# Performance work log

Measured on AMD Instinct MI355X. Metric: run time of the kernel, lower is better.

## Reference

```python
import jax, jax.numpy as jnp
import numpy as np

N = 50000      # num_nodes
E = 800000     # edges (before self loops)
IN = 64        # in_dim
H = 128        # hidden_node_dim
DH = 256       # decoder_and_message_hidden_dim
L = 3          # propagation_steps


def _lin(key, fan_in, fan_out):
    s = 1.0 / np.sqrt(fan_in)
    return jax.random.uniform(key, (fan_in, fan_out), jnp.float32, -s, s)


def setup_inputs() -> dict:
    key = jax.random.key(0)
    ks = iter(jax.random.split(key, 40))
    x = jax.random.normal(next(ks), (N, IN), jnp.float32)
    edge_index = jax.random.randint(next(ks), (2, E), 0, N, jnp.int64)
    enc_W = _lin(next(ks), IN, H); enc_b = jnp.zeros((H,), jnp.float32)
    # message MLP: Linear(2H->DH) tanh, Linear(DH->DH) tanh, Linear(DH->H)
    msg_W0 = jnp.stack([_lin(next(ks), 2 * H, DH) for _ in range(L)])
    msg_b0 = jnp.zeros((L, DH), jnp.float32)
    msg_W1 = jnp.stack([_lin(next(ks), DH, DH) for _ in range(L)])
    msg_b1 = jnp.zeros((L, DH), jnp.float32)
    msg_W2 = jnp.stack([_lin(next(ks), DH, H) for _ in range(L)])
    msg_b2 = jnp.zeros((L, H), jnp.float32)
    # GRUCell params, torch layout [3H, H] chunks (r, z, n)
    gru_Wih = jnp.stack([_lin(next(ks), H, 3 * H).T for _ in range(L)])
    gru_Whh = jnp.stack([_lin(next(ks), H, 3 * H).T for _ in range(L)])
    gru_bih = jnp.zeros((L, 3 * H), jnp.float32)
    gru_bhh = jnp.zeros((L, 3 * H), jnp.float32)
    # decoder: Linear(H->DH) tanh, Linear(DH->DH) tanh, Linear(DH->1)
    dec_W0 = _lin(next(ks), H, DH); dec_b0 = jnp.zeros((DH,), jnp.float32)
    dec_W1 = _lin(next(ks), DH, DH); dec_b1 = jnp.zeros((DH,), jnp.float32)
    dec_W2 = _lin(next(ks), DH, 1); dec_b2 = jnp.zeros((1,), jnp.float32)
    return dict(x=x, edge_index=edge_index, enc_W=enc_W, enc_b=enc_b,
                msg_W0=msg_W0, msg_b0=msg_b0, msg_W1=msg_W1, msg_b1=msg_b1,
                msg_W2=msg_W2, msg_b2=msg_b2, gru_Wih=gru_Wih, gru_Whh=gru_Whh,
                gru_bih=gru_bih, gru_bhh=gru_bhh, dec_W0=dec_W0, dec_b0=dec_b0,
                dec_W1=dec_W1, dec_b1=dec_b1, dec_W2=dec_W2, dec_b2=dec_b2)


def reference(x, edge_index, enc_W, enc_b, msg_W0, msg_b0, msg_W1, msg_b1,
              msg_W2, msg_b2, gru_Wih, gru_Whh, gru_bih, gru_bhh,
              dec_W0, dec_b0, dec_W1, dec_b1, dec_W2, dec_b2):
    n = x.shape[0]
    # add self loops (PyG add_self_loops appends (v, v))
    loops = jnp.arange(n, dtype=edge_index.dtype)
    src = jnp.concatenate([edge_index[0], loops])  # j (source)
    dst = jnp.concatenate([edge_index[1], loops])  # i (target)
    counts = jax.ops.segment_sum(jnp.ones_like(dst, jnp.float32), dst, num_segments=n)
    h = jnp.tanh(x @ enc_W + enc_b)                # encoder [N, H]
    for l in range(L):
        # message: f([x_i || x_j]) per edge
        m = jnp.concatenate([h[dst], h[src]], axis=-1)            # [E+N, 2H]
        m = jnp.tanh(m @ msg_W0[l] + msg_b0[l])
        m = jnp.tanh(m @ msg_W1[l] + msg_b1[l])
        m = m @ msg_W2[l] + msg_b2[l]                              # [E+N, H]
        aggr = jax.ops.segment_sum(m, dst, num_segments=n) / counts[:, None]
        # GRUCell(input=aggr, hidden=h)
        gi = aggr @ gru_Wih[l].T + gru_bih[l]                      # [N, 3H]
        gh = h @ gru_Whh[l].T + gru_bhh[l]
        i_r, i_z, i_n = jnp.split(gi, 3, axis=-1)
        h_r, h_z, h_n = jnp.split(gh, 3, axis=-1)
        r = jax.nn.sigmoid(i_r + h_r)
        z = jax.nn.sigmoid(i_z + h_z)
        nn_ = jnp.tanh(i_n + r * h_n)
        h = (1.0 - z) * nn_ + z * h
    # decoder
    y = jnp.tanh(h @ dec_W0 + dec_b0)
    y = jnp.tanh(y @ dec_W1 + dec_b1)
    y = y @ dec_W2 + dec_b2                                        # [N, 1]
    return y.reshape(-1, n)[0]                                     # view(-1, N).squeeze(0)
```

## Files before the change

### kernel.cpp

```cpp
#include <hip/hip_runtime.h>

typedef __bf16 bf16x8 __attribute__((ext_vector_type(8)));
typedef float  f32x4  __attribute__((ext_vector_type(4)));

__device__ inline unsigned short f2bf(float f){
  __bf16 b = (__bf16)f;
  return __builtin_bit_cast(unsigned short, b);
}
__device__ inline unsigned int pack2bf(float lo, float hi){
  return (unsigned)f2bf(lo) | ((unsigned)f2bf(hi) << 16);
}
__device__ inline float tanh_fast(float x){
  float e = __builtin_amdgcn_exp2f(x * 2.8853900817779268f);
  return 1.0f - 2.0f * __builtin_amdgcn_rcpf(e + 1.0f);
}
__device__ inline float sigmoid_fast(float x){
  float e = __builtin_amdgcn_exp2f(x * -1.4426950408889634f);
  return __builtin_amdgcn_rcpf(1.0f + e);
}
__device__ inline float bflo(unsigned int u){ return __uint_as_float(u << 16); }
__device__ inline float bfhi(unsigned int u){ return __uint_as_float(u & 0xffff0000u); }

__device__ __forceinline__ void bar_nodrain(){
  asm volatile("s_waitcnt lgkmcnt(0)" ::: "memory");
  __builtin_amdgcn_s_barrier();
}

__device__ inline int nthbit(unsigned long long m, int n){
  for (int k = 0; k < n; k++) m &= m - 1;
  return m ? (int)__builtin_ctzll(m) : 0;
}

__global__ void k_count(const int* __restrict__ ei, int* __restrict__ cnt, int E){
  int e = blockIdx.x * 256 + threadIdx.x;
  if (e < E) atomicAdd(&cnt[ei[E + e]], 1);
}

__global__ __launch_bounds__(1024) void k_scan(const int* __restrict__ cnt, int* __restrict__ cursor, int N){
  __shared__ int partial[1024];
  int t = threadIdx.x;
  int chunk = (N + 1023) / 1024;
  int lo = t * chunk, hi = min(lo + chunk, N);
  int s = 0;
  for (int v = lo; v < hi; v++) s += cnt[v] + 1;
  partial[t] = s;
  __syncthreads();
  for (int off = 1; off < 1024; off <<= 1){
    int val = (t >= off) ? partial[t - off] : 0;
    __syncthreads();
    partial[t] += val;
    __syncthreads();
  }
  int base = (t == 0) ? 0 : partial[t - 1];
  for (int v = lo; v < hi; v++){ cursor[v] = base; base += cnt[v] + 1; }
}

__global__ void k_scatter(const int* __restrict__ ei, int* __restrict__ cursor,
                          int* __restrict__ srcS, int* __restrict__ dstS, int E, int N){
  int i = blockIdx.x * 256 + threadIdx.x;
  int Et = E + N;
  if (i >= Et) return;
  int s, d;
  if (i < E){ s = ei[i]; d = ei[E + i]; } else { s = d = i - E; }
  int pos = atomicAdd(&cursor[d], 1);
  srcS[pos] = s; dstS[pos] = d;
}

__global__ void k_wprep(const float* __restrict__ msgW1, const float* __restrict__ msgW2,
                        unsigned short* __restrict__ W1T, unsigned short* __restrict__ W2T){
  int idx = blockIdx.x * 256 + threadIdx.x;
  if (idx < 3 * 256 * 256){
    int l = idx >> 16, r = idx & 65535; int n = r >> 8, k = r & 255;
    W1T[idx] = f2bf(msgW1[(size_t)l * 65536 + k * 256 + n]);
  }
  int i2 = idx - 3 * 65536;
  if (i2 >= 0 && i2 < 3 * 128 * 256){
    int l = i2 >> 15, r = i2 & 32767; int hh = r >> 8, k = r & 255;
    W2T[i2] = f2bf(msgW2[(size_t)l * 32768 + k * 128 + hh]);
  }
}

__global__ void k_wprep2(const float* __restrict__ msgW0, unsigned short* __restrict__ W0T){
  int idx = blockIdx.x * 256 + threadIdx.x;
  if (idx >= 3 * 2 * 256 * 128) return;
  int l = idx / 65536, r = idx % 65536;
  int half = r >> 15, r2 = r & 32767, c = r2 >> 7, k = r2 & 127;
  W0T[idx] = f2bf(msgW0[(size_t)l * 65536 + (half * 128 + k) * 256 + c]);
}

__global__ void k_wprep3(const float* __restrict__ gWih, const float* __restrict__ gWhh,
                         unsigned short* __restrict__ Wcat){
  int idx = blockIdx.x * 256 + threadIdx.x;
  if (idx >= 3 * 384 * 256) return;
  int l = idx / 98304, r = idx % 98304, j = r >> 8, k = r & 255;
  float v = (k < 128) ? gWih[((size_t)l * 384 + j) * 128 + k]
                      : gWhh[((size_t)l * 384 + j) * 128 + (k - 128)];
  Wcat[idx] = f2bf(v);
}

__global__ void k_wprep4(const float* __restrict__ encW, const float* __restrict__ dW0,
                         const float* __restrict__ dW1,
                         const float* __restrict__ gbih, const float* __restrict__ gbhh,
                         unsigned short* __restrict__ encWT, unsigned short* __restrict__ dW0T,
                         unsigned short* __restrict__ dW1T,
                         float* __restrict__ brz, float* __restrict__ bin, float* __restrict__ bhn){
  int idx = blockIdx.x * 256 + threadIdx.x;
  if (idx < 8192){ int c = idx >> 6, k = idx & 63; encWT[idx] = f2bf(encW[k * 128 + c]); return; }
  idx -= 8192;
  if (idx < 32768){ int c = idx >> 7, k = idx & 127; dW0T[idx] = f2bf(dW0[k * 256 + c]); return; }
  idx -= 32768;
  if (idx < 65536){ int c = idx >> 8, k = idx & 255; dW1T[idx] = f2bf(dW1[k * 256 + c]); return; }
  idx -= 65536;
  if (idx < 768){ int l = idx >> 8, j = idx & 255; brz[idx] = gbih[l * 384 + j] + gbhh[l * 384 + j]; return; }
  idx -= 768;
  if (idx < 384){ int l = idx >> 7, j = idx & 127; bin[idx] = gbih[l * 384 + 256 + j]; return; }
  idx -= 384;
  if (idx < 384){ int l = idx >> 7, j = idx & 127; bhn[idx] = gbhh[l * 384 + 256 + j]; return; }
}

__global__ __launch_bounds__(256) void k_enc(const float* __restrict__ x,
        const unsigned short* __restrict__ encWT, const float* __restrict__ encb,
        float* __restrict__ h, unsigned short* __restrict__ hb, int N){
  __shared__ __align__(16) unsigned char xb[64 * 128];
  int n0 = blockIdx.x * 64, t = threadIdx.x;
  #pragma unroll
  for (int p = 0; p < 2; p++){
    int i = t + p * 256;
    int row = i >> 3, ch = i & 7;
    int node = n0 + row;
    unsigned int o[4] = {0,0,0,0};
    if (node < N){
      const float* s = x + (size_t)node * 64 + ch * 8;
      float4 a = *(const float4*)s, b = *(const float4*)(s + 4);
      o[0] = pack2bf(a.x, a.y);
      o[1] = pack2bf(a.z, a.w);
      o[2] = pack2bf(b.x, b.y);
      o[3] = pack2bf(b.z, b.w);
    }
    *(uint4*)(xb + row * 128 + ((ch * 16) ^ ((row & 7) << 4))) = make_uint4(o[0], o[1], o[2], o[3]);
  }
  __syncthreads();
  int wv = t >> 6, lane = t & 63, l15 = lane & 15, kg = lane >> 4;
  int c32 = wv * 32;
  f32x4 acc[2][4];
  #pragma unroll
  for (int ct = 0; ct < 2; ct++){
    int c = c32 + ct * 16 + kg * 4;
    float4 be = *(const float4*)(encb + c);
    f32x4 binit = {be.x, be.y, be.z, be.w};
    #pragma unroll
    for (int b_ = 0; b_ < 4; b_++) acc[ct][b_] = binit;
  }
  const unsigned char* wp = (const unsigned char*)encWT;
  #pragma unroll
  for (int ks = 0; ks < 2; ks++){
    int koff = ks * 64 + kg * 16;
    bf16x8 bfr[4], afr[2];
    #pragma unroll
    for (int nt = 0; nt < 4; nt++){
      int row = nt * 16 + l15;
      bfr[nt] = *(const bf16x8*)(xb + row * 128 + (koff ^ ((row & 7) << 4)));
    }
    #pragma unroll
    for (int ct = 0; ct < 2; ct++)
      afr[ct] = *(const bf16x8*)(wp + (size_t)(c32 + ct * 16 + l15) * 128 + koff);
    #pragma unroll
    for (int ct = 0; ct < 2; ct++)
      #pragma unroll
      for (int nt = 0; nt < 4; nt++)
        acc[ct][nt] = __builtin_amdgcn_mfma_f32_16x16x32_bf16(afr[ct], bfr[nt], acc[ct][nt], 0, 0, 0);
  }
  #pragma unroll
  for (int ct = 0; ct < 2; ct++){
    int c = c32 + ct * 16 + kg * 4;
    #pragma unroll
    for (int nt = 0; nt < 4; nt++){
      int node = n0 + nt * 16 + l15;
      if (node >= N) continue;
      f32x4 v = acc[ct][nt];
      float o0 = tanh_fast(v[0]), o1 = tanh_fast(v[1]);
      float o2 = tanh_fast(v[2]), o3 = tanh_fast(v[3]);
      float4 fo; fo.x = o0; fo.y = o1; fo.z = o2; fo.w = o3;
      *(float4*)(h + (size_t)node * 128 + c) = fo;
      uint2 bo; bo.x = pack2bf(o0, o1); bo.y = pack2bf(o2, o3);
      *(uint2*)(hb + (size_t)node * 128 + c) = bo;
    }
  }
}

__global__ __launch_bounds__(256) void k_ab(const unsigned short* __restrict__ hb,
        const unsigned short* __restrict__ W0T, const float* __restrict__ b0,
        unsigned short* __restrict__ A, unsigned short* __restrict__ B, int N){
  __shared__ __align__(16) unsigned char ub[64 * 256];
  int n0 = blockIdx.x * 64, t = threadIdx.x;
  #pragma unroll
  for (int p = 0; p < 4; p++){
    int i = t + p * 256;
    int row = i >> 4, ch = i & 15;
    int node = n0 + row;
    uint4 v = (node < N) ? *(const uint4*)(hb + (size_t)node * 128 + ch * 8) : make_uint4(0,0,0,0);
    *(uint4*)(ub + row * 256 + ((ch * 16) ^ ((row & 7) << 4))) = v;
  }
  __syncthreads();
  int wv = t >> 6, lane = t & 63, l15 = lane & 15, kg = lane >> 4;
  f32x4 zero = {0.f, 0.f, 0.f, 0.f};
  int c64 = wv * 64;
  f32x4 accA[4][4], accB[4][4];
  #pragma unroll
  for (int ct = 0; ct < 4; ct++){
    int c = c64 + ct * 16 + kg * 4;
    float4 b4 = *(const float4*)(b0 + c);
    f32x4 binit = {b4.x, b4.y, b4.z, b4.w};
    #pragma unroll
    for (int b_ = 0; b_ < 4; b_++){ accA[ct][b_] = binit; accB[ct][b_] = zero; }
  }
  const unsigned char* wa = (const unsigned char*)W0T;
  const unsigned char* wb = wa + 65536;
  #pragma unroll
  for (int ks = 0; ks < 4; ks++){
    int koff = ks * 64 + kg * 16;
    bf16x8 bfr[4];
    #pragma unroll
    for (int nt = 0; nt < 4; nt++){
      int row = nt * 16 + l15;
      bfr[nt] = *(const bf16x8*)(ub + row * 256 + (koff ^ ((row & 7) << 4)));
    }
    bf16x8 afA[4], afB[4];
    #pragma unroll
    for (int ct = 0; ct < 4; ct++){
      int r = c64 + ct * 16 + l15;
      afA[ct] = *(const bf16x8*)(wa + (size_t)r * 256 + koff);
      afB[ct] = *(const bf16x8*)(wb + (size_t)r * 256 + koff);
    }
    #pragma unroll
    for (int ct = 0; ct < 4; ct++)
      #pragma unroll
      for (int nt = 0; nt < 4; nt++){
        accA[ct][nt] = __builtin_amdgcn_mfma_f32_16x16x32_bf16(afA[ct], bfr[nt], accA[ct][nt], 0, 0, 0);
        accB[ct][nt] = __builtin_amdgcn_mfma_f32_16x16x32_bf16(afB[ct], bfr[nt], accB[ct][nt], 0, 0, 0);
      }
  }
  #pragma unroll
  for (int ct = 0; ct < 4; ct++){
    int c = c64 + ct * 16 + kg * 4;
    #pragma unroll
    for (int nt = 0; nt < 4; nt++){
      int node = n0 + nt * 16 + l15;
      if (node >= N) continue;
      f32x4 va = accA[ct][nt], vb = accB[ct][nt];
      uint2 oa, ob;
      oa.x = pack2bf(va[0], va[1]); oa.y = pack2bf(va[2], va[3]);
      ob.x = pack2bf(vb[0], vb[1]); ob.y = pack2bf(vb[2], vb[3]);
      *(uint2*)(A + (size_t)node * 256 + c) = oa;
      *(uint2*)(B + (size_t)node * 256 + c) = ob;
    }
  }
}

__global__ __launch_bounds__(256, 4) void k_edge(
        const int* __restrict__ srcS, const int* __restrict__ dstS,
        const unsigned short* __restrict__ Abuf, const unsigned short* __restrict__ Bbuf,
        const unsigned short* __restrict__ W1T, const unsigned short* __restrict__ W2T,
        const float* __restrict__ b1, const float* __restrict__ b2,
        float* __restrict__ aggr){
  __shared__ __align__(16) unsigned char lds[40960];
  unsigned char* t0  = lds;
  unsigned char* t1q = lds + 32768;
  int t = threadIdx.x;
  int wv = t >> 6, lane = t & 63, l15 = lane & 15, kg = lane >> 4;
  int e0 = blockIdx.x * 64;

  int sv = srcS[e0 + lane];
  int dv = dstS[e0 + lane];

  int chunk = lane & 31;
  int rbase = wv * 2 + (lane >> 5);
  uint4 av[8], bv[8];
  #pragma unroll
  for (int p = 0; p < 8; p++){
    int row = p * 8 + rbase;
    int d = __shfl(dv, row), s = __shfl(sv, row);
    if (d >= 0){
      av[p] = *(const uint4*)(Abuf + (size_t)d * 256 + chunk * 8);
      bv[p] = *(const uint4*)(Bbuf + (size_t)s * 256 + chunk * 8);
    } else { av[p] = make_uint4(0,0,0,0); bv[p] = make_uint4(0,0,0,0); }
  }

  int prevd = __shfl(dv, (lane == 0) ? 0 : (lane - 1));
  bool valid = (dv >= 0);
  bool flag  = valid && (lane == 0 || prevd != dv);
  unsigned long long sm  = __ballot(flag);
  unsigned long long ivm = __ballot(!valid);
  int nseg   = (int)__popcll(sm);
  int endAll = 64 - (int)__popcll(ivm);

  int segSt, segEn, segD;
  {
    int st_ = nthbit(sm, lane);
    int en_ = (lane + 1 < nseg) ? nthbit(sm, lane + 1) : endAll;
    segSt = st_; segEn = en_;
    segD  = __shfl(dv, st_);
  }

  #pragma unroll
  for (int p = 0; p < 8; p++){
    int r = p * 8 + rbase;
    unsigned int o[4]; unsigned int ua, ub;
    ua = av[p].x; ub = bv[p].x;
    o[0] = pack2bf(tanh_fast(bflo(ua)+bflo(ub)), tanh_fast(bfhi(ua)+bfhi(ub)));
    ua = av[p].y; ub = bv[p].y;
    o[1] = pack2bf(tanh_fast(bflo(ua)+bflo(ub)), tanh_fast(bfhi(ua)+bfhi(ub)));
    ua = av[p].z; ub = bv[p].z;
    o[2] = pack2bf(tanh_fast(bflo(ua)+bflo(ub)), tanh_fast(bfhi(ua)+bfhi(ub)));
    ua = av[p].w; ub = bv[p].w;
    o[3] = pack2bf(tanh_fast(bflo(ua)+bflo(ub)), tanh_fast(bfhi(ua)+bfhi(ub)));
    *(uint4*)(t0 + r * 512 + ((chunk * 16) ^ ((r & 7) << 4))) = make_uint4(o[0],o[1],o[2],o[3]);
  }
  bar_nodrain();

  const unsigned char* w1b = (const unsigned char*)W1T;
  const unsigned char* w2b = (const unsigned char*)W2T;
  int hbase = wv * 32;

  f32x4 acc2[2][4];
  #pragma unroll
  for (int ht = 0; ht < 2; ht++){
    int hb_ = hbase + ht * 16 + kg * 4;
    float4 c4 = *(const float4*)(b2 + hb_);
    f32x4 binit = {c4.x, c4.y, c4.z, c4.w};
    #pragma unroll
    for (int b_ = 0; b_ < 4; b_++) acc2[ht][b_] = binit;
  }

  #pragma unroll
  for (int pass = 0; pass < 4; pass++){
    {
      int nbase = pass * 64 + wv * 16;
      f32x4 acc[4];
      {
        int ng = nbase + kg * 4;
        float4 c4 = *(const float4*)(b1 + ng);
        f32x4 binit = {c4.x, c4.y, c4.z, c4.w};
        #pragma unroll
        for (int b_ = 0; b_ < 4; b_++) acc[b_] = binit;
      }
      #pragma unroll
      for (int ks = 0; ks < 8; ks++){
        int koff = ks * 64 + kg * 16;
        bf16x8 afr = *(const bf16x8*)(w1b + (size_t)(nbase + l15) * 512 + koff);
        bf16x8 bfr[4];
        #pragma unroll
        for (int et = 0; et < 4; et++){
          int row = et * 16 + l15;
          bfr[et] = *(const bf16x8*)(t0 + row * 512 + (koff ^ ((row & 7) << 4)));
        }
        #pragma unroll
        for (int et = 0; et < 4; et++)
          acc[et] = __builtin_amdgcn_mfma_f32_16x16x32_bf16(afr, bfr[et], acc[et], 0, 0, 0);
      }
      int nl2 = (wv * 16 + kg * 4) * 2;
      #pragma unroll
      for (int et = 0; et < 4; et++){
        int edge = et * 16 + l15;
        f32x4 v = acc[et];
        unsigned int p0 = pack2bf(tanh_fast(v[0]), tanh_fast(v[1]));
        unsigned int p1 = pack2bf(tanh_fast(v[2]), tanh_fast(v[3]));
        *(uint2*)(t1q + edge * 128 + (nl2 ^ ((edge & 7) << 4))) = make_uint2(p0, p1);
      }
    }
    bar_nodrain();

    #pragma unroll
    for (int ks = 0; ks < 2; ks++){
      int koff  = ks * 64 + kg * 16;
      int wkoff = pass * 128 + koff;
      bf16x8 afr[2], bfr[4];
      #pragma unroll
      for (int ht = 0; ht < 2; ht++)
        afr[ht] = *(const bf16x8*)(w2b + (size_t)(hbase + ht * 16 + l15) * 512 + wkoff);
      #pragma unroll
      for (int et = 0; et < 4; et++){
        int row = et * 16 + l15;
        bfr[et] = *(const bf16x8*)(t1q + row * 128 + (koff ^ ((row & 7) << 4)));
      }
      #pragma unroll
      for (int ht = 0; ht < 2; ht++)
        #pragma unroll
        for (int et = 0; et < 4; et++)
          acc2[ht][et] = __builtin_amdgcn_mfma_f32_16x16x32_bf16(afr[ht], bfr[et], acc2[ht][et], 0, 0, 0);
    }
    bar_nodrain();
  }

  #pragma unroll
  for (int ht = 0; ht < 2; ht++){
    int hb_ = hbase + ht * 16 + kg * 4;
    int cch = hb_ >> 2;
    #pragma unroll
    for (int et = 0; et < 4; et++){
      int edge = et * 16 + l15;
      f32x4 v = acc2[ht][et];
      float4 o; o.x = v[0]; o.y = v[1]; o.z = v[2]; o.w = v[3];
      *(float4*)(t0 + edge * 512 + ((cch ^ (edge & 7)) << 4)) = o;
    }
  }
  bar_nodrain();

  {
    int c = lane & 31;
    int sstr = wv * 2 + (lane >> 5);
    #pragma unroll
    for (int s0 = 0; s0 < 8; s0++){
      int s = sstr + s0 * 8;
      int st = __shfl(segSt, s);
      int en = __shfl(segEn, s);
      int d  = __shfl(segD,  s);
      if (s < nseg){
        float4 sum; sum.x = sum.y = sum.z = sum.w = 0.f;
        for (int e = st; e < en; e++){
          float4 v = *(const float4*)(t0 + e * 512 + ((c ^ (e & 7)) << 4));
          sum.x += v.x; sum.y += v.y; sum.z += v.z; sum.w += v.w;
        }
        float* base = aggr + (size_t)d * 128 + c * 4;
        atomicAdd(base + 0, sum.x);
        atomicAdd(base + 1, sum.y);
        atomicAdd(base + 2, sum.z);
        atomicAdd(base + 3, sum.w);
      }
    }
  }
}

__global__ __launch_bounds__(256) void k_gru(const float* __restrict__ aggr, const int* __restrict__ cnt,
    float* __restrict__ h, unsigned short* __restrict__ hb,
    const unsigned short* __restrict__ Wcat, const float* __restrict__ brz,
    const float* __restrict__ bin, const float* __restrict__ bhn, int N){
  __shared__ __align__(16) unsigned char u[64 * 512];
  __shared__ __align__(16) unsigned char hf[64 * 512];
  int n0 = blockIdx.x * 64, t = threadIdx.x;
  {
    int row = t >> 2, node = n0 + row;
    int q4 = t & 3;
    bool isA = q4 < 2;
    float inv = 0.f;
    if (isA && node < N) inv = __builtin_amdgcn_rcpf((float)(cnt[node] + 1));
    #pragma unroll
    for (int p = 0; p < 8; p++){
      int ch = q4 * 8 + p;
      unsigned int o[4] = {0,0,0,0};
      if (node < N){
        if (isA){
          const float* s = aggr + (size_t)node * 128 + ch * 8;
          float4 a = *(const float4*)s, b = *(const float4*)(s + 4);
          a.x *= inv; a.y *= inv; a.z *= inv; a.w *= inv;
          b.x *= inv; b.y *= inv; b.z *= inv; b.w *= inv;
          o[0] = pack2bf(a.x, a.y); o[1] = pack2bf(a.z, a.w);
          o[2] = pack2bf(b.x, b.y); o[3] = pack2bf(b.z, b.w);
        } else {
          const float* s = h + (size_t)node * 128 + (ch - 16) * 8;
          float4 a = *(const float4*)s, b = *(const float4*)(s + 4);
          o[0] = pack2bf(a.x, a.y); o[1] = pack2bf(a.z, a.w);
          o[2] = pack2bf(b.x, b.y); o[3] = pack2bf(b.z, b.w);
          int c2 = (ch - 16) * 2;
          *(float4*)(hf + row * 512 + ((c2 * 16) ^ ((row & 7) << 4))) = a;
          *(float4*)(hf + row * 512 + (((c2 + 1) * 16) ^ ((row & 7) << 4))) = b;
        }
      }
      *(uint4*)(u + row * 512 + ((ch * 16) ^ ((row & 7) << 4))) = make_uint4(o[0], o[1], o[2], o[3]);
    }
  }
  __syncthreads();
  int wv = t >> 6, lane = t & 63, l15 = lane & 15, kg = lane >> 4;
  int j32 = wv * 32;
  f32x4 accR[2][4], accZ[2][4], accI[2][4], accH[2][4];
  #pragma unroll
  for (int jt = 0; jt < 2; jt++){
    int j = j32 + jt * 16 + kg * 4;
    float4 br = *(const float4*)(brz + j);
    float4 bz = *(const float4*)(brz + 128 + j);
    float4 bi = *(const float4*)(bin + j);
    float4 bh = *(const float4*)(bhn + j);
    f32x4 vr = {br.x, br.y, br.z, br.w};
    f32x4 vz = {bz.x, bz.y, bz.z, bz.w};
    f32x4 vi = {bi.x, bi.y, bi.z, bi.w};
    f32x4 vh = {bh.x, bh.y, bh.z, bh.w};
    #pragma unroll
    for (int b_ = 0; b_ < 4; b_++){ accR[jt][b_] = vr; accZ[jt][b_] = vz; accI[jt][b_] = vi; accH[jt][b_] = vh; }
  }
  const unsigned char* wc = (const unsigned char*)Wcat;
  #pragma unroll
  for (int ks = 0; ks < 8; ks++){
    int koff = ks * 64 + kg * 16;
    bf16x8 bfr[4];
    #pragma unroll
    for (int nt = 0; nt < 4; nt++){
      int row = nt * 16 + l15;
      bfr[nt] = *(const bf16x8*)(u + row * 512 + (koff ^ ((row & 7) << 4)));
    }
    bf16x8 aR[2], aZ[2], aN[2];
    #pragma unroll
    for (int jt = 0; jt < 2; jt++){
      int jr = j32 + jt * 16 + l15;
      aR[jt] = *(const bf16x8*)(wc + (size_t)jr * 512 + koff);
      aZ[jt] = *(const bf16x8*)(wc + (size_t)(128 + jr) * 512 + koff);
      aN[jt] = *(const bf16x8*)(wc + (size_t)(256 + jr) * 512 + koff);
    }
    #pragma unroll
    for (int jt = 0; jt < 2; jt++)
      #pragma unroll
      for (int nt = 0; nt < 4; nt++){
        accR[jt][nt] = __builtin_amdgcn_mfma_f32_16x16x32_bf16(aR[jt], bfr[nt], accR[jt][nt], 0, 0, 0);
        accZ[jt][nt] = __builtin_amdgcn_mfma_f32_16x16x32_bf16(aZ[jt], bfr[nt], accZ[jt][nt], 0, 0, 0);
      }
    if (ks < 4){
      #pragma unroll
      for (int jt = 0; jt < 2; jt++)
        #pragma unroll
        for (int nt = 0; nt < 4; nt++)
          accI[jt][nt] = __builtin_amdgcn_mfma_f32_16x16x32_bf16(aN[jt], bfr[nt], accI[jt][nt], 0, 0, 0);
    } else {
      #pragma unroll
      for (int jt = 0; jt < 2; jt++)
        #pragma unroll
        for (int nt = 0; nt < 4; nt++)
          accH[jt][nt] = __builtin_amdgcn_mfma_f32_16x16x32_bf16(aN[jt], bfr[nt], accH[jt][nt], 0, 0, 0);
    }
  }
  #pragma unroll
  for (int jt = 0; jt < 2; jt++){
    int j = j32 + jt * 16 + kg * 4;
    #pragma unroll
    for (int nt = 0; nt < 4; nt++){
      int rloc = nt * 16 + l15;
      int node = n0 + rloc;
      if (node >= N) continue;
      float4 hold = *(const float4*)(hf + rloc * 512 + ((j * 4) ^ ((rloc & 7) << 4)));
      f32x4 vr = accR[jt][nt], vz = accZ[jt][nt], vi = accI[jt][nt], vh = accH[jt][nt];
      float o[4];
      {
        float r0 = sigmoid_fast(vr[0]), z0 = sigmoid_fast(vz[0]);
        o[0] = (1.f - z0) * tanh_fast(vi[0] + r0 * vh[0]) + z0 * hold.x;
        float r1 = sigmoid_fast(vr[1]), z1 = sigmoid_fast(vz[1]);
        o[1] = (1.f - z1) * tanh_fast(vi[1] + r1 * vh[1]) + z1 * hold.y;
        float r2 = sigmoid_fast(vr[2]), z2 = sigmoid_fast(vz[2]);
        o[2] = (1.f - z2) * tanh_fast(vi[2] + r2 * vh[2]) + z2 * hold.z;
        float r3 = sigmoid_fast(vr[3]), z3 = sigmoid_fast(vz[3]);
        o[3] = (1.f - z3) * tanh_fast(vi[3] + r3 * vh[3]) + z3 * hold.w;
      }
      float4 fo; fo.x = o[0]; fo.y = o[1]; fo.z = o[2]; fo.w = o[3];
      *(float4*)(h + (size_t)node * 128 + j) = fo;
      uint2 bo; bo.x = pack2bf(o[0], o[1]); bo.y = pack2bf(o[2], o[3]);
      *(uint2*)(hb + (size_t)node * 128 + j) = bo;
    }
  }
}

__global__ __launch_bounds__(256) void k_dec(const unsigned short* __restrict__ hb,
    const unsigned short* __restrict__ dW0T, const float* __restrict__ db0,
    const unsigned short* __restrict__ dW1T, const float* __restrict__ db1,
    const float* __restrict__ dW2, const float* __restrict__ db2,
    float* __restrict__ out, int N){
  __shared__ __align__(16) unsigned char ub[64 * 256];
  __shared__ __align__(16) unsigned char y1[64 * 512];
  __shared__ __align__(16) unsigned char y2[64 * 1024];
  int n0 = blockIdx.x * 64, t = threadIdx.x;
  #pragma unroll
  for (int p = 0; p < 4; p++){
    int i = t + p * 256;
    int row = i >> 4, ch = i & 15;
    int node = n0 + row;
    uint4 v = (node < N) ? *(const uint4*)(hb + (size_t)node * 128 + ch * 8) : make_uint4(0,0,0,0);
    *(uint4*)(ub + row * 256 + ((ch * 16) ^ ((row & 7) << 4))) = v;
  }
  __syncthreads();
  int wv = t >> 6, lane = t & 63, l15 = lane & 15, kg = lane >> 4;
  int c64 = wv * 64;
  {
    f32x4 acc[4][4];
    #pragma unroll
    for (int ct = 0; ct < 4; ct++){
      int c = c64 + ct * 16 + kg * 4;
      float4 b4 = *(const float4*)(db0 + c);
      f32x4 binit = {b4.x, b4.y, b4.z, b4.w};
      #pragma unroll
      for (int b_ = 0; b_ < 4; b_++) acc[ct][b_] = binit;
    }
    const unsigned char* wp = (const unsigned char*)dW0T;
    #pragma unroll
    for (int ks = 0; ks < 4; ks++){
      int koff = ks * 64 + kg * 16;
      bf16x8 bfr[4], afr[4];
      #pragma unroll
      for (int nt = 0; nt < 4; nt++){
        int row = nt * 16 + l15;
        bfr[nt] = *(const bf16x8*)(ub + row * 256 + (koff ^ ((row & 7) << 4)));
      }
      #pragma unroll
      for (int ct = 0; ct < 4; ct++)
        afr[ct] = *(const bf16x8*)(wp + (size_t)(c64 + ct * 16 + l15) * 256 + koff);
      #pragma unroll
      for (int ct = 0; ct < 4; ct++)
        #pragma unroll
        for (int nt = 0; nt < 4; nt++)
          acc[ct][nt] = __builtin_amdgcn_mfma_f32_16x16x32_bf16(afr[ct], bfr[nt], acc[ct][nt], 0, 0, 0);
    }
    #pragma unroll
    for (int ct = 0; ct < 4; ct++){
      int c = c64 + ct * 16 + kg * 4;
      #pragma unroll
      for (int nt = 0; nt < 4; nt++){
        int row = nt * 16 + l15;
        f32x4 v = acc[ct][nt];
        unsigned int p0 = pack2bf(tanh_fast(v[0]), tanh_fast(v[1]));
        unsigned int p1 = pack2bf(tanh_fast(v[2]), tanh_fast(v[3]));
        *(uint2*)(y1 + row * 512 + ((c * 2) ^ ((row & 7) << 4))) = make_uint2(p0, p1);
      }
    }
  }
  __syncthreads();
  {
    f32x4 acc[4][4];
    #pragma unroll
    for (int ct = 0; ct < 4; ct++){
      int c = c64 + ct * 16 + kg * 4;
      float4 b4 = *(const float4*)(db1 + c);
      f32x4 binit = {b4.x, b4.y, b4.z, b4.w};
      #pragma unroll
      for (int b_ = 0; b_ < 4; b_++) acc[ct][b_] = binit;
    }
    const unsigned char* wp = (const unsigned char*)dW1T;
    #pragma unroll
    for (int ks = 0; ks < 8; ks++){
      int koff = ks * 64 + kg * 16;
      bf16x8 bfr[4], afr[4];
      #pragma unroll
      for (int nt = 0; nt < 4; nt++){
        int row = nt * 16 + l15;
        bfr[nt] = *(const bf16x8*)(y1 + row * 512 + (koff ^ ((row & 7) << 4)));
      }
      #pragma unroll
      for (int ct = 0; ct < 4; ct++)
        afr[ct] = *(const bf16x8*)(wp + (size_t)(c64 + ct * 16 + l15) * 512 + koff);
      #pragma unroll
      for (int ct = 0; ct < 4; ct++)
        #pragma unroll
        for (int nt = 0; nt < 4; nt++)
          acc[ct][nt] = __builtin_amdgcn_mfma_f32_16x16x32_bf16(afr[ct], bfr[nt], acc[ct][nt], 0, 0, 0);
    }
    #pragma unroll
    for (int ct = 0; ct < 4; ct++){
      int c = c64 + ct * 16 + kg * 4;
      #pragma unroll
      for (int nt = 0; nt < 4; nt++){
        int row = nt * 16 + l15;
        f32x4 v = acc[ct][nt];
        float4 o;
        o.x = tanh_fast(v[0]); o.y = tanh_fast(v[1]);
        o.z = tanh_fast(v[2]); o.w = tanh_fast(v[3]);
        *(float4*)(y2 + row * 1024 + ((c * 4) ^ ((row & 7) << 4))) = o;
      }
    }
  }
  __syncthreads();
  {
    int node = t >> 2, part = t & 3;
    float p = 0.f;
    #pragma unroll
    for (int q = 0; q < 16; q++){
      int c = part * 64 + q * 4;
      float4 v = *(const float4*)(y2 + node * 1024 + ((c * 4) ^ ((node & 7) << 4)));
      float4 w = *(const float4*)(dW2 + c);
      p += v.x * w.x + v.y * w.y + v.z * w.z + v.w * w.w;
    }
    p += __shfl_down(p, 2, 4);
    p += __shfl_down(p, 1, 4);
    if (part == 0 && (n0 + node) < N) out[n0 + node] = p + db2[0];
  }
}

extern "C" void kernel_launch(void* const* d_in, const int* in_sizes, int n_in,
                              void* d_out, int out_size, void* d_ws, size_t ws_size,
                              hipStream_t stream){
  const float* x     = (const float*)d_in[0];
  const int*   ei    = (const int*)  d_in[1];
  const float* encW  = (const float*)d_in[2];
  const float* encb  = (const float*)d_in[3];
  const float* msgW0 = (const float*)d_in[4];
  const float* msgb0 = (const float*)d_in[5];
  const float* msgW1 = (const float*)d_in[6];
  const float* msgb1 = (const float*)d_in[7];
  const float* msgW2 = (const float*)d_in[8];
  const float* msgb2 = (const float*)d_in[9];
  const float* gWih  = (const float*)d_in[10];
  const float* gWhh  = (const float*)d_in[11];
  const float* gbih  = (const float*)d_in[12];
  const float* gbhh  = (const float*)d_in[13];
  const float* dW0   = (const float*)d_in[14];
  const float* db0   = (const float*)d_in[15];
  const float* dW1   = (const float*)d_in[16];
  const float* db1   = (const float*)d_in[17];
  const float* dW2   = (const float*)d_in[18];
  const float* db2   = (const float*)d_in[19];
  int N = in_sizes[0] / 64;
  int E = in_sizes[1] / 2;
  float* out = (float*)d_out;

  int Et = E + N;
  int EtPad = (Et + 63) & ~63;

  char* ws = (char*)d_ws;
  size_t off = 0;
  auto alloc = [&](size_t bytes)->void*{
    void* p = ws + off; off += (bytes + 255) & ~(size_t)255; return p;
  };
  float*          h      = (float*)         alloc((size_t)N * 128 * 4);
  unsigned short* hbuf   = (unsigned short*)alloc((size_t)N * 128 * 2);
  unsigned short* Abuf   = (unsigned short*)alloc((size_t)N * 256 * 2);
  unsigned short* Bbuf   = (unsigned short*)alloc((size_t)N * 256 * 2);
  float*          aggr   = (float*)         alloc((size_t)N * 128 * 4);
  int*            cnt    = (int*)           alloc((size_t)N * 4);
  int*            cursor = (int*)           alloc((size_t)N * 4);
  int*            srcS   = (int*)           alloc((size_t)EtPad * 4);
  int*            dstS   = (int*)           alloc((size_t)EtPad * 4);
  unsigned short* W1T    = (unsigned short*)alloc((size_t)3 * 65536 * 2);
  unsigned short* W2T    = (unsigned short*)alloc((size_t)3 * 32768 * 2);
  unsigned short* W0T    = (unsigned short*)alloc((size_t)3 * 65536 * 2);
  unsigned short* Wcat   = (unsigned short*)alloc((size_t)3 * 98304 * 2);
  unsigned short* encWT  = (unsigned short*)alloc((size_t)8192 * 2);
  unsigned short* dW0T   = (unsigned short*)alloc((size_t)32768 * 2);
  unsigned short* dW1T   = (unsigned short*)alloc((size_t)65536 * 2);
  float*          brz    = (float*)         alloc((size_t)768 * 4);
  float*          binb   = (float*)         alloc((size_t)384 * 4);
  float*          bhnb   = (float*)         alloc((size_t)384 * 4);
  (void)ws_size; (void)n_in; (void)out_size;

  hipMemsetAsync(cnt, 0, (size_t)N * 4, stream);
  hipMemsetAsync(dstS, 0xFF, (size_t)EtPad * 4, stream);
  k_count<<<(E + 255) / 256, 256, 0, stream>>>(ei, cnt, E);
  k_scan<<<1, 1024, 0, stream>>>(cnt, cursor, N);
  k_scatter<<<(Et + 255) / 256, 256, 0, stream>>>(ei, cursor, srcS, dstS, E, N);
  k_wprep<<<(3 * 65536 + 3 * 32768 + 255) / 256, 256, 0, stream>>>(msgW1, msgW2, W1T, W2T);
  k_wprep2<<<(3 * 65536 + 255) / 256, 256, 0, stream>>>(msgW0, W0T);
  k_wprep3<<<(3 * 98304 + 255) / 256, 256, 0, stream>>>(gWih, gWhh, Wcat);
  k_wprep4<<<(108032 + 255) / 256, 256, 0, stream>>>(encW, dW0, dW1, gbih, gbhh,
                                                     encWT, dW0T, dW1T, brz, binb, bhnb);

  int nb64 = (N + 63) / 64;
  k_enc<<<nb64, 256, 0, stream>>>(x, encWT, encb, h, hbuf, N);

  int eb = EtPad / 64;
  for (int l = 0; l < 3; l++){
    k_ab<<<nb64, 256, 0, stream>>>(hbuf, W0T + (size_t)l * 65536, msgb0 + (size_t)l * 256,
                                   Abuf, Bbuf, N);
    hipMemsetAsync(aggr, 0, (size_t)N * 128 * 4, stream);
    k_edge<<<eb, 256, 0, stream>>>(srcS, dstS, Abuf, Bbuf,
        W1T + (size_t)l * 65536, W2T + (size_t)l * 32768,
        msgb1 + (size_t)l * 256, msgb2 + (size_t)l * 128,
        aggr);
    k_gru<<<nb64, 256, 0, stream>>>(aggr, cnt, h, hbuf,
        Wcat + (size_t)l * 98304, brz + (size_t)l * 256,
        binb + (size_t)l * 128, bhnb + (size_t)l * 128, N);
  }
  k_dec<<<nb64, 256, 0, stream>>>(hbuf, dW0T, db0, dW1T, db1, dW2, db2, out, N);
}
```

Baseline: 1.527 ms.

## Fuse per-node message first-layer projection into encoder and GRU kernels

The separate k_ab launch, which reloads the bf16 hidden state from global memory and computes the per-node A/B projections for the next layer's message MLP, is removed. Its work now runs at the end of k_enc and k_gru on the freshly computed hidden tile, which is kept in LDS in swizzled layout. This saves three kernel launches and the global reread of hbuf. In exchange the encoder and GRU kernels use more LDS and registers, which may lower occupancy, and they gain extra barriers.

```diff
diff --git a/kernel.cpp b/kernel.cpp
--- a/kernel.cpp
+++ b/kernel.cpp
@@ -118,11 +118,75 @@
   if (idx < 384){ int l = idx >> 7, j = idx & 127; bhn[idx] = gbhh[l * 384 + 256 + j]; return; }
 }
 
+__device__ __forceinline__ void ab_body(const unsigned char* hn,
+        const unsigned short* __restrict__ W0T, const float* __restrict__ b0,
+        unsigned short* __restrict__ A, unsigned short* __restrict__ B,
+        int n0, int N, int wv, int l15, int kg){
+  f32x4 zero = {0.f, 0.f, 0.f, 0.f};
+  int c64 = wv * 64;
+  f32x4 accA[4][4], accB[4][4];
+  #pragma unroll
+  for (int ct = 0; ct < 4; ct++){
+    int c = c64 + ct * 16 + kg * 4;
+    float4 b4 = *(const float4*)(b0 + c);
+    f32x4 binit = {b4.x, b4.y, b4.z, b4.w};
+    #pragma unroll
+    for (int b_ = 0; b_ < 4; b_++){ accA[ct][b_] = binit; accB[ct][b_] = zero; }
+  }
+  const unsigned char* wa = (const unsigned char*)W0T;
+  const unsigned char* wb = wa + 65536;
+  #pragma unroll
+  for (int ks = 0; ks < 4; ks++){
+    int koff = ks * 64 + kg * 16;
+    bf16x8 bfr[4];
+    #pragma unroll
+    for (int nt = 0; nt < 4; nt++){
+      int row = nt * 16 + l15;
+      bfr[nt] = *(const bf16x8*)(hn + row * 256 + (koff ^ ((row & 7) << 4)));
+    }
+    bf16x8 afA[4], afB[4];
+    #pragma unroll
+    for (int ct = 0; ct < 4; ct++){
+      int r = c64 + ct * 16 + l15;
+      afA[ct] = *(const bf16x8*)(wa + (size_t)r * 256 + koff);
+      afB[ct] = *(const bf16x8*)(wb + (size_t)r * 256 + koff);
+    }
+    #pragma unroll
+    for (int ct = 0; ct < 4; ct++)
+      #pragma unroll
+      for (int nt = 0; nt < 4; nt++){
+        accA[ct][nt] = __builtin_amdgcn_mfma_f32_16x16x32_bf16(afA[ct], bfr[nt], accA[ct][nt], 0, 0, 0);
+        accB[ct][nt] = __builtin_amdgcn_mfma_f32_16x16x32_bf16(afB[ct], bfr[nt], accB[ct][nt], 0, 0, 0);
+      }
+  }
+  #pragma unroll
+  for (int ct = 0; ct < 4; ct++){
+    int c = c64 + ct * 16 + kg * 4;
+    #pragma unroll
+    for (int nt = 0; nt < 4; nt++){
+      int node = n0 + nt * 16 + l15;
+      if (node >= N) continue;
+      f32x4 va = accA[ct][nt], vb = accB[ct][nt];
+      uint2 oa, ob;
+      oa.x = pack2bf(va[0], va[1]); oa.y = pack2bf(va[2], va[3]);
+      ob.x = pack2bf(vb[0], vb[1]); ob.y = pack2bf(vb[2], vb[3]);
+      *(uint2*)(A + (size_t)node * 256 + c) = oa;
+      *(uint2*)(B + (size_t)node * 256 + c) = ob;
+    }
+  }
+}
+
 __global__ __launch_bounds__(256) void k_enc(const float* __restrict__ x,
         const unsigned short* __restrict__ encWT, const float* __restrict__ encb,
-        float* __restrict__ h, unsigned short* __restrict__ hb, int N){
+        const unsigned short* __restrict__ W0T0, const float* __restrict__ b00,
+        float* __restrict__ h, unsigned short* __restrict__ hb,
+        unsigned short* __restrict__ A, unsigned short* __restrict__ B, int N){
   __shared__ __align__(16) unsigned char xb[64 * 128];
+  __shared__ __align__(16) unsigned char hn[64 * 256];
   int n0 = blockIdx.x * 64, t = threadIdx.x;
+  #pragma unroll
+  for (int i = 0; i < 4; i++)
+    *(uint4*)(hn + (t + i * 256) * 16) = make_uint4(0, 0, 0, 0);
   #pragma unroll
   for (int p = 0; p < 2; p++){
     int i = t + p * 256;
@@ -175,7 +239,8 @@
     int c = c32 + ct * 16 + kg * 4;
     #pragma unroll
     for (int nt = 0; nt < 4; nt++){
-      int node = n0 + nt * 16 + l15;
+      int row = nt * 16 + l15;
+      int node = n0 + row;
       if (node >= N) continue;
       f32x4 v = acc[ct][nt];
       float o0 = tanh_fast(v[0]), o1 = tanh_fast(v[1]);
@@ -184,77 +249,11 @@
       *(float4*)(h + (size_t)node * 128 + c) = fo;
       uint2 bo; bo.x = pack2bf(o0, o1); bo.y = pack2bf(o2, o3);
       *(uint2*)(hb + (size_t)node * 128 + c) = bo;
-    }
-  }
-}
-
-__global__ __launch_bounds__(256) void k_ab(const unsigned short* __restrict__ hb,
-        const unsigned short* __restrict__ W0T, const float* __restrict__ b0,
-        unsigned short* __restrict__ A, unsigned short* __restrict__ B, int N){
-  __shared__ __align__(16) unsigned char ub[64 * 256];
-  int n0 = blockIdx.x * 64, t = threadIdx.x;
-  #pragma unroll
-  for (int p = 0; p < 4; p++){
-    int i = t + p * 256;
-    int row = i >> 4, ch = i & 15;
-    int node = n0 + row;
-    uint4 v = (node < N) ? *(const uint4*)(hb + (size_t)node * 128 + ch * 8) : make_uint4(0,0,0,0);
-    *(uint4*)(ub + row * 256 + ((ch * 16) ^ ((row & 7) << 4))) = v;
+      *(uint2*)(hn + row * 256 + ((((c >> 3) << 4) ^ ((row & 7) << 4)) + ((c & 7) << 1))) = bo;
+    }
   }
   __syncthreads();
-  int wv = t >> 6, lane = t & 63, l15 = lane & 15, kg = lane >> 4;
-  f32x4 zero = {0.f, 0.f, 0.f, 0.f};
-  int c64 = wv * 64;
-  f32x4 accA[4][4], accB[4][4];
-  #pragma unroll
-  for (int ct = 0; ct < 4; ct++){
-    int c = c64 + ct * 16 + kg * 4;
-    float4 b4 = *(const float4*)(b0 + c);
-    f32x4 binit = {b4.x, b4.y, b4.z, b4.w};
-    #pragma unroll
-    for (int b_ = 0; b_ < 4; b_++){ accA[ct][b_] = binit; accB[ct][b_] = zero; }
-  }
-  const unsigned char* wa = (const unsigned char*)W0T;
-  const unsigned char* wb = wa + 65536;
-  #pragma unroll
-  for (int ks = 0; ks < 4; ks++){
-    int koff = ks * 64 + kg * 16;
-    bf16x8 bfr[4];
-    #pragma unroll
-    for (int nt = 0; nt < 4; nt++){
-      int row = nt * 16 + l15;
-      bfr[nt] = *(const bf16x8*)(ub + row * 256 + (koff ^ ((row & 7) << 4)));
-    }
-    bf16x8 afA[4], afB[4];
-    #pragma unroll
-    for (int ct = 0; ct < 4; ct++){
-      int r = c64 + ct * 16 + l15;
-      afA[ct] = *(const bf16x8*)(wa + (size_t)r * 256 + koff);
-      afB[ct] = *(const bf16x8*)(wb + (size_t)r * 256 + koff);
-    }
-    #pragma unroll
-    for (int ct = 0; ct < 4; ct++)
-      #pragma unroll
-      for (int nt = 0; nt < 4; nt++){
-        accA[ct][nt] = __builtin_amdgcn_mfma_f32_16x16x32_bf16(afA[ct], bfr[nt], accA[ct][nt], 0, 0, 0);
-        accB[ct][nt] = __builtin_amdgcn_mfma_f32_16x16x32_bf16(afB[ct], bfr[nt], accB[ct][nt], 0, 0, 0);
-      }
-  }
-  #pragma unroll
-  for (int ct = 0; ct < 4; ct++){
-    int c = c64 + ct * 16 + kg * 4;
-    #pragma unroll
-    for (int nt = 0; nt < 4; nt++){
-      int node = n0 + nt * 16 + l15;
-      if (node >= N) continue;
-      f32x4 va = accA[ct][nt], vb = accB[ct][nt];
-      uint2 oa, ob;
-      oa.x = pack2bf(va[0], va[1]); oa.y = pack2bf(va[2], va[3]);
-      ob.x = pack2bf(vb[0], vb[1]); ob.y = pack2bf(vb[2], vb[3]);
-      *(uint2*)(A + (size_t)node * 256 + c) = oa;
-      *(uint2*)(B + (size_t)node * 256 + c) = ob;
-    }
-  }
+  ab_body(hn, W0T0, b00, A, B, n0, N, wv, l15, kg);
 }
 
 __global__ __launch_bounds__(256, 4) void k_edge(
@@ -434,7 +433,9 @@
 __global__ __launch_bounds__(256) void k_gru(const float* __restrict__ aggr, const int* __restrict__ cnt,
     float* __restrict__ h, unsigned short* __restrict__ hb,
     const unsigned short* __restrict__ Wcat, const float* __restrict__ brz,
-    const float* __restrict__ bin, const float* __restrict__ bhn, int N){
+    const float* __restrict__ bin, const float* __restrict__ bhn,
+    int doAB, const unsigned short* __restrict__ W0Tn, const float* __restrict__ b0n,
+    unsigned short* __restrict__ A, unsigned short* __restrict__ B, int N){
   __shared__ __align__(16) unsigned char u[64 * 512];
   __shared__ __align__(16) unsigned char hf[64 * 512];
   int n0 = blockIdx.x * 64, t = threadIdx.x;
@@ -526,6 +527,7 @@
           accH[jt][nt] = __builtin_amdgcn_mfma_f32_16x16x32_bf16(aN[jt], bfr[nt], accH[jt][nt], 0, 0, 0);
     }
   }
+  __syncthreads();
   #pragma unroll
   for (int jt = 0; jt < 2; jt++){
     int j = j32 + jt * 16 + kg * 4;
@@ -551,7 +553,12 @@
       *(float4*)(h + (size_t)node * 128 + j) = fo;
       uint2 bo; bo.x = pack2bf(o[0], o[1]); bo.y = pack2bf(o[2], o[3]);
       *(uint2*)(hb + (size_t)node * 128 + j) = bo;
-    }
+      *(uint2*)(u + rloc * 256 + ((((j >> 3) << 4) ^ ((rloc & 7) << 4)) + ((j & 7) << 1))) = bo;
+    }
+  }
+  if (doAB){
+    __syncthreads();
+    ab_body(u, W0Tn, b0n, A, B, n0, N, wv, l15, kg);
   }
 }
 
@@ -746,20 +753,21 @@
                                                      encWT, dW0T, dW1T, brz, binb, bhnb);
 
   int nb64 = (N + 63) / 64;
-  k_enc<<<nb64, 256, 0, stream>>>(x, encWT, encb, h, hbuf, N);
+  k_enc<<<nb64, 256, 0, stream>>>(x, encWT, encb, W0T, msgb0, h, hbuf, Abuf, Bbuf, N);
 
   int eb = EtPad / 64;
   for (int l = 0; l < 3; l++){
-    k_ab<<<nb64, 256, 0, stream>>>(hbuf, W0T + (size_t)l * 65536, msgb0 + (size_t)l * 256,
-                                   Abuf, Bbuf, N);
     hipMemsetAsync(aggr, 0, (size_t)N * 128 * 4, stream);
     k_edge<<<eb, 256, 0, stream>>>(srcS, dstS, Abuf, Bbuf,
         W1T + (size_t)l * 65536, W2T + (size_t)l * 32768,
         msgb1 + (size_t)l * 256, msgb2 + (size_t)l * 128,
         aggr);
+    int nl = (l < 2) ? (l + 1) : 2;
     k_gru<<<nb64, 256, 0, stream>>>(aggr, cnt, h, hbuf,
         Wcat + (size_t)l * 98304, brz + (size_t)l * 256,
-        binb + (size_t)l * 128, bhnb + (size_t)l * 128, N);
+        binb + (size_t)l * 128, bhnb + (size_t)l * 128,
+        (l < 2) ? 1 : 0, W0T + (size_t)nl * 65536, msgb0 + (size_t)nl * 256,
+        Abuf, Bbuf, N);
   }
   k_dec<<<nb64, 256, 0, stream>>>(hbuf, dW0T, db0, dW1T, db1, dW2, db2, out, N);
 }
```

After: 1.543 ms. No clear change (+1.1%).
